# Kernel optimization log

Measured on AMD Instinct MI355X. Metric: run time of the kernel, lower is better.

## Reference

```python
import jax, jax.numpy as jnp
import numpy as np

DEPTH = 11  # tree depth -> depth+1 routing steps, n_nodes = 2**(DEPTH+1)-1 = 4095


def setup_inputs() -> dict:
    key = jax.random.key(0)
    k1, k2, k3 = jax.random.split(key, 3)
    B, D_in, D_out = 8192, 2048, 2048
    n_nodes = 2 ** (DEPTH + 1) - 1
    x = jax.random.normal(k1, (B, D_in), dtype=jnp.float32)
    # nn.Linear(input_width, n_nodes, bias=False).weight : (n_nodes, D_in)
    W_in = jax.random.normal(k2, (n_nodes, D_in), dtype=jnp.float32) / np.sqrt(D_in).astype(np.float32)
    # nn.Linear(n_nodes, output_width, bias=False).weight : (D_out, n_nodes)
    W_out = jax.random.normal(k3, (D_out, n_nodes), dtype=jnp.float32) / np.sqrt(n_nodes).astype(np.float32)
    return {"x": x, "W_in": W_in, "W_out": W_out}


def reference(x, W_in, W_out):
    B = x.shape[0]
    # Torch loop recomputes linear_in(x) every step; the result is identical each
    # iteration, so compute the (B, n_nodes) logits once and gather per depth step.
    logits_all = x @ W_in.T  # (B, n_nodes)

    def step(cur, _):
        # gather the logit of each sample's current tree node
        score = jnp.take_along_axis(logits_all, cur[:, None], axis=1)[:, 0]  # (B,)
        nxt = cur * 2 + (score >= 0).astype(jnp.int32) + 1  # left/right child
        return nxt, (cur, score)

    init = jnp.zeros((B,), dtype=jnp.int32)
    _, (nodes, scores) = jax.lax.scan(step, init, None, length=DEPTH + 1)
    nodes = nodes.T    # (B, depth+1) visited node ids
    scores = scores.T  # (B, depth+1) selected logits

    mlp1 = jax.nn.gelu(scores, approximate=False)  # exact GELU, matches nn.GELU
    # Conditional output projection: only the depth+1 visited columns of W_out
    # contribute per sample (FFF / conditional-MoE semantics).
    W_sel = W_out.T[nodes]  # (B, depth+1, D_out)
    return jnp.einsum('bd,bdo->bo', mlp1, W_sel)
```

## Files before the change

### kernel.cpp

```cpp
#include <hip/hip_runtime.h>
#include <math.h>

#define B_SZ     8192
#define D_IN     2048
#define D_OUT    2048
#define N_NODES  4095
#define STEPS    12
#define N_LEAVES 2048
#define N_SUB    512
#define CAP      64

typedef float f4_t __attribute__((ext_vector_type(4)));

__device__ __forceinline__ float4 nt_load4(const float* p) {
  f4_t v = __builtin_nontemporal_load((const f4_t*)p);
  return make_float4(v.x, v.y, v.z, v.w);
}

__global__ __launch_bounds__(256) void transpose_wout(
    const float* __restrict__ W, float* __restrict__ Wt) {
  __shared__ float tile[64][65];
  const int bx = blockIdx.x;
  const int tid = threadIdx.x;
  const int col0 = (bx & 63) * 64;
  const int row0 = (bx >> 6) * 64;
  const int r  = tid >> 4;
  const int c4 = (tid & 15) * 4;

  #pragma unroll
  for (int i = 0; i < 4; ++i) {
    const int row = r + i * 16;
    const float* src = W + (size_t)(row0 + row) * N_NODES + col0 + c4;
    if (col0 + c4 + 3 < N_NODES) {
      const float4 v = nt_load4(src);
      tile[c4 + 0][row] = v.x; tile[c4 + 1][row] = v.y;
      tile[c4 + 2][row] = v.z; tile[c4 + 3][row] = v.w;
    } else {
      #pragma unroll
      for (int k = 0; k < 4; ++k)
        tile[c4 + k][row] = (col0 + c4 + k < N_NODES) ? src[k] : 0.0f;
    }
  }
  __syncthreads();
  #pragma unroll
  for (int i = 0; i < 4; ++i) {
    const int rn = r + i * 16;
    const int node = col0 + rn;
    if (node < N_NODES) {
      float4 v;
      v.x = tile[rn][c4 + 0]; v.y = tile[rn][c4 + 1];
      v.z = tile[rn][c4 + 2]; v.w = tile[rn][c4 + 3];
      *(float4*)(Wt + (size_t)node * D_OUT + row0 + c4) = v;
    }
  }
}

__global__ __launch_bounds__(256) void route_kernel(
    const float* __restrict__ x, const float* __restrict__ W_in,
    int* __restrict__ cnt, int* __restrict__ bucket,
    float* __restrict__ gsc) {
  const int wave = (int)((blockIdx.x * (size_t)blockDim.x + threadIdx.x) >> 6);
  const int lane = threadIdx.x & 63;
  if (wave >= B_SZ) return;

  const float* xbase = x + (size_t)wave * D_IN;
  float4 xv0 = nt_load4(xbase + (lane + 0 * 64) * 4);
  float4 xv1 = nt_load4(xbase + (lane + 1 * 64) * 4);
  float4 xv2 = nt_load4(xbase + (lane + 2 * 64) * 4);
  float4 xv3 = nt_load4(xbase + (lane + 3 * 64) * 4);
  float4 xv4 = nt_load4(xbase + (lane + 4 * 64) * 4);
  float4 xv5 = nt_load4(xbase + (lane + 5 * 64) * 4);
  float4 xv6 = nt_load4(xbase + (lane + 6 * 64) * 4);
  float4 xv7 = nt_load4(xbase + (lane + 7 * 64) * 4);

  int cur = 0;
  #pragma unroll
  for (int d = 0; d < STEPS; ++d) {
    const float4* wr = (const float4*)(W_in + (size_t)cur * D_IN);
    const float4 w0 = wr[lane + 0 * 64];
    const float4 w1 = wr[lane + 1 * 64];
    const float4 w2 = wr[lane + 2 * 64];
    const float4 w3 = wr[lane + 3 * 64];
    const float4 w4 = wr[lane + 4 * 64];
    const float4 w5 = wr[lane + 5 * 64];
    const float4 w6 = wr[lane + 6 * 64];
    const float4 w7 = wr[lane + 7 * 64];
    float s = 0.0f;
    s += xv0.x * w0.x + xv0.y * w0.y + xv0.z * w0.z + xv0.w * w0.w;
    s += xv1.x * w1.x + xv1.y * w1.y + xv1.z * w1.z + xv1.w * w1.w;
    s += xv2.x * w2.x + xv2.y * w2.y + xv2.z * w2.z + xv2.w * w2.w;
    s += xv3.x * w3.x + xv3.y * w3.y + xv3.z * w3.z + xv3.w * w3.w;
    s += xv4.x * w4.x + xv4.y * w4.y + xv4.z * w4.z + xv4.w * w4.w;
    s += xv5.x * w5.x + xv5.y * w5.y + xv5.z * w5.z + xv5.w * w5.w;
    s += xv6.x * w6.x + xv6.y * w6.y + xv6.z * w6.z + xv6.w * w6.w;
    s += xv7.x * w7.x + xv7.y * w7.y + xv7.z * w7.z + xv7.w * w7.w;

    #pragma unroll
    for (int off = 32; off > 0; off >>= 1) s += __shfl_xor(s, off);

    if (lane == 0) {
      gsc[wave * STEPS + d] = 0.5f * s * (1.0f + erff(s * 0.70710678118654752f));
      if (d == STEPS - 1) {
        const int leaf = cur - 2047;
        const int pos = atomicAdd(&cnt[leaf], 1);
        if (pos < CAP) bucket[leaf * CAP + pos] = wave;
      }
    }
    cur = cur * 2 + ((s >= 0.0f) ? 2 : 1);
  }
}

__global__ __launch_bounds__(256) void out_kernel(
    const float* __restrict__ Wt, const int* __restrict__ cnt,
    const int* __restrict__ bucket, const float* __restrict__ gsc,
    float* __restrict__ out) {
  const int sub = blockIdx.x * 4 + (threadIdx.x >> 6);
  const int lane = threadIdx.x & 63;
  const int col = blockIdx.y * 64 + lane;

  int anc[10];
  {
    int nd = 511 + sub;
    #pragma unroll
    for (int d = 9; d >= 0; --d) { anc[d] = nd; nd = (nd - 1) >> 1; }
  }
  const int p10a = 1023 + 2 * sub;
  const int leaf0n = 2047 + 4 * sub;

  float wa[10], wp[2], wl[4];
  #pragma unroll
  for (int d = 0; d < 10; ++d)
    wa[d] = Wt[(size_t)anc[d] * D_OUT + col];
  #pragma unroll
  for (int k = 0; k < 2; ++k)
    wp[k] = Wt[(size_t)(p10a + k) * D_OUT + col];
  #pragma unroll
  for (int k = 0; k < 4; ++k)
    wl[k] = Wt[(size_t)(leaf0n + k) * D_OUT + col];

  int n0 = cnt[4 * sub + 0]; if (n0 > CAP) n0 = CAP;
  int n1 = cnt[4 * sub + 1]; if (n1 > CAP) n1 = CAP;
  int n2 = cnt[4 * sub + 2]; if (n2 > CAP) n2 = CAP;
  int n3 = cnt[4 * sub + 3]; if (n3 > CAP) n3 = CAP;
  const int p1 = n0, p2 = n0 + n1, p3 = n0 + n1 + n2;
  const int total = p3 + n3;

  for (int base = 0; base < total; base += 64) {
    const int m = (total - base < 64) ? (total - base) : 64;
    int packed = 0;
    {
      const int gi = base + lane;
      if (gi < total) {
        int lc, off;
        if      (gi < p1) { lc = 0; off = 0;  }
        else if (gi < p2) { lc = 1; off = p1; }
        else if (gi < p3) { lc = 2; off = p2; }
        else              { lc = 3; off = p3; }
        const int b = bucket[(4 * sub + lc) * CAP + (gi - off)];
        packed = (lc << 28) | b;
      }
    }
    int pA = __shfl(packed, 0);
    int pB = __shfl(packed, (m > 1) ? 1 : 0);
    const float4* gA = (const float4*)(gsc + (size_t)(pA & 0x0FFFFFFF) * STEPS);
    float4 a0 = gA[0], a1 = gA[1], a2 = gA[2];
    const float4* gB = (const float4*)(gsc + (size_t)(pB & 0x0FFFFFFF) * STEPS);
    float4 b0 = gB[0], b1 = gB[1], b2 = gB[2];

    for (int j = 0; j < m; ++j) {
      int jn = j + 2; if (jn >= m) jn = m - 1;
      const int pC = __shfl(packed, jn);
      const float4* gC = (const float4*)(gsc + (size_t)(pC & 0x0FFFFFFF) * STEPS);
      const float4 t0 = gC[0], t1 = gC[1], t2 = gC[2];

      const int b  = pA & 0x0FFFFFFF;
      const int lc = pA >> 28;
      const float w10 = (lc & 2) ? wp[1] : wp[0];
      const float w11 = (lc & 2) ? ((lc & 1) ? wl[3] : wl[2])
                                 : ((lc & 1) ? wl[1] : wl[0]);
      float acc;
      acc  = a0.x * wa[0];
      acc += a0.y * wa[1];
      acc += a0.z * wa[2];
      acc += a0.w * wa[3];
      acc += a1.x * wa[4];
      acc += a1.y * wa[5];
      acc += a1.z * wa[6];
      acc += a1.w * wa[7];
      acc += a2.x * wa[8];
      acc += a2.y * wa[9];
      acc += a2.z * w10;
      acc += a2.w * w11;
      __builtin_nontemporal_store(acc, out + (size_t)b * D_OUT + col);

      pA = pB; a0 = b0; a1 = b1; a2 = b2;
      pB = pC; b0 = t0; b1 = t1; b2 = t2;
    }
  }
}

extern "C" void kernel_launch(void* const* d_in, const int* in_sizes, int n_in,
                              void* d_out, int out_size, void* d_ws, size_t ws_size,
                              hipStream_t stream) {
  const float* x     = (const float*)d_in[0];
  const float* W_in  = (const float*)d_in[1];
  const float* W_out = (const float*)d_in[2];
  float* out = (float*)d_out;

  char* p = (char*)d_ws;
  float* Wt     = (float*)p;  p += (size_t)N_NODES * D_OUT * sizeof(float);
  int*   cnt    = (int*)p;    p += (size_t)N_LEAVES * sizeof(int);
  int*   bucket = (int*)p;    p += (size_t)N_LEAVES * CAP * sizeof(int);
  float* gsc    = (float*)p;

  hipMemsetAsync(cnt, 0, (size_t)N_LEAVES * sizeof(int), stream);

  route_kernel<<<dim3(B_SZ / 4), dim3(256), 0, stream>>>(
      x, W_in, cnt, bucket, gsc);

  transpose_wout<<<dim3(2048), dim3(256), 0, stream>>>(W_out, Wt);

  out_kernel<<<dim3(N_SUB / 4, 32), dim3(256), 0, stream>>>(
      Wt, cnt, bucket, gsc, out);
}
```

Measured before the change: 245.5 us.

## Vectorize out_kernel to four columns per lane and pin loads with asm barriers

The output kernel now has each lane handle four adjacent columns, using float4 weight loads and float4 nontemporal stores. This cuts the grid's y dimension by four and amortizes the per-sample gsc loads and shuffles over more work. The routing kernel gains a launch_bounds occupancy hint and empty asm barriers that force the x and W_in loads to be issued early. The transpose drops its nontemporal hint on W_out loads. The price is higher register pressure in out_kernel and fewer blocks overall.

```diff
diff --git a/kernel.cpp b/kernel.cpp
--- a/kernel.cpp
+++ b/kernel.cpp
@@ -10,11 +10,10 @@
 #define N_SUB    512
 #define CAP      64
 
-typedef float f4_t __attribute__((ext_vector_type(4)));
-
-__device__ __forceinline__ float4 nt_load4(const float* p) {
-  f4_t v = __builtin_nontemporal_load((const f4_t*)p);
-  return make_float4(v.x, v.y, v.z, v.w);
+typedef float f4 __attribute__((ext_vector_type(4)));
+
+__device__ __forceinline__ f4 nt_load(const float* p) {
+  return __builtin_nontemporal_load((const f4*)p);
 }
 
 __global__ __launch_bounds__(256) void transpose_wout(
@@ -32,7 +31,7 @@
     const int row = r + i * 16;
     const float* src = W + (size_t)(row0 + row) * N_NODES + col0 + c4;
     if (col0 + c4 + 3 < N_NODES) {
-      const float4 v = nt_load4(src);
+      const float4 v = *(const float4*)src;
       tile[c4 + 0][row] = v.x; tile[c4 + 1][row] = v.y;
       tile[c4 + 2][row] = v.z; tile[c4 + 3][row] = v.w;
     } else {
@@ -55,7 +54,7 @@
   }
 }
 
-__global__ __launch_bounds__(256) void route_kernel(
+__global__ __launch_bounds__(256, 5) void route_kernel(
     const float* __restrict__ x, const float* __restrict__ W_in,
     int* __restrict__ cnt, int* __restrict__ bucket,
     float* __restrict__ gsc) {
@@ -64,27 +63,31 @@
   if (wave >= B_SZ) return;
 
   const float* xbase = x + (size_t)wave * D_IN;
-  float4 xv0 = nt_load4(xbase + (lane + 0 * 64) * 4);
-  float4 xv1 = nt_load4(xbase + (lane + 1 * 64) * 4);
-  float4 xv2 = nt_load4(xbase + (lane + 2 * 64) * 4);
-  float4 xv3 = nt_load4(xbase + (lane + 3 * 64) * 4);
-  float4 xv4 = nt_load4(xbase + (lane + 4 * 64) * 4);
-  float4 xv5 = nt_load4(xbase + (lane + 5 * 64) * 4);
-  float4 xv6 = nt_load4(xbase + (lane + 6 * 64) * 4);
-  float4 xv7 = nt_load4(xbase + (lane + 7 * 64) * 4);
+  f4 xv0 = nt_load(xbase + (lane + 0 * 64) * 4);
+  f4 xv1 = nt_load(xbase + (lane + 1 * 64) * 4);
+  f4 xv2 = nt_load(xbase + (lane + 2 * 64) * 4);
+  f4 xv3 = nt_load(xbase + (lane + 3 * 64) * 4);
+  f4 xv4 = nt_load(xbase + (lane + 4 * 64) * 4);
+  f4 xv5 = nt_load(xbase + (lane + 5 * 64) * 4);
+  f4 xv6 = nt_load(xbase + (lane + 6 * 64) * 4);
+  f4 xv7 = nt_load(xbase + (lane + 7 * 64) * 4);
+  asm volatile("" : "+v"(xv0), "+v"(xv1), "+v"(xv2), "+v"(xv3),
+                    "+v"(xv4), "+v"(xv5), "+v"(xv6), "+v"(xv7));
 
   int cur = 0;
   #pragma unroll
   for (int d = 0; d < STEPS; ++d) {
-    const float4* wr = (const float4*)(W_in + (size_t)cur * D_IN);
-    const float4 w0 = wr[lane + 0 * 64];
-    const float4 w1 = wr[lane + 1 * 64];
-    const float4 w2 = wr[lane + 2 * 64];
-    const float4 w3 = wr[lane + 3 * 64];
-    const float4 w4 = wr[lane + 4 * 64];
-    const float4 w5 = wr[lane + 5 * 64];
-    const float4 w6 = wr[lane + 6 * 64];
-    const float4 w7 = wr[lane + 7 * 64];
+    const f4* wr = (const f4*)(W_in + (size_t)cur * D_IN);
+    f4 w0 = wr[lane + 0 * 64];
+    f4 w1 = wr[lane + 1 * 64];
+    f4 w2 = wr[lane + 2 * 64];
+    f4 w3 = wr[lane + 3 * 64];
+    f4 w4 = wr[lane + 4 * 64];
+    f4 w5 = wr[lane + 5 * 64];
+    f4 w6 = wr[lane + 6 * 64];
+    f4 w7 = wr[lane + 7 * 64];
+    asm volatile("" : "+v"(w0), "+v"(w1), "+v"(w2), "+v"(w3),
+                      "+v"(w4), "+v"(w5), "+v"(w6), "+v"(w7));
     float s = 0.0f;
     s += xv0.x * w0.x + xv0.y * w0.y + xv0.z * w0.z + xv0.w * w0.w;
     s += xv1.x * w1.x + xv1.y * w1.y + xv1.z * w1.z + xv1.w * w1.w;
@@ -116,7 +119,7 @@
     float* __restrict__ out) {
   const int sub = blockIdx.x * 4 + (threadIdx.x >> 6);
   const int lane = threadIdx.x & 63;
-  const int col = blockIdx.y * 64 + lane;
+  const int col = blockIdx.y * 256 + lane * 4;
 
   int anc[10];
   {
@@ -127,16 +130,26 @@
   const int p10a = 1023 + 2 * sub;
   const int leaf0n = 2047 + 4 * sub;
 
-  float wa[10], wp[2], wl[4];
-  #pragma unroll
-  for (int d = 0; d < 10; ++d)
-    wa[d] = Wt[(size_t)anc[d] * D_OUT + col];
-  #pragma unroll
-  for (int k = 0; k < 2; ++k)
-    wp[k] = Wt[(size_t)(p10a + k) * D_OUT + col];
-  #pragma unroll
-  for (int k = 0; k < 4; ++k)
-    wl[k] = Wt[(size_t)(leaf0n + k) * D_OUT + col];
+  f4 wa0 = *(const f4*)(Wt + (size_t)anc[0] * D_OUT + col);
+  f4 wa1 = *(const f4*)(Wt + (size_t)anc[1] * D_OUT + col);
+  f4 wa2 = *(const f4*)(Wt + (size_t)anc[2] * D_OUT + col);
+  f4 wa3 = *(const f4*)(Wt + (size_t)anc[3] * D_OUT + col);
+  f4 wa4 = *(const f4*)(Wt + (size_t)anc[4] * D_OUT + col);
+  f4 wa5 = *(const f4*)(Wt + (size_t)anc[5] * D_OUT + col);
+  f4 wa6 = *(const f4*)(Wt + (size_t)anc[6] * D_OUT + col);
+  f4 wa7 = *(const f4*)(Wt + (size_t)anc[7] * D_OUT + col);
+  f4 wa8 = *(const f4*)(Wt + (size_t)anc[8] * D_OUT + col);
+  f4 wa9 = *(const f4*)(Wt + (size_t)anc[9] * D_OUT + col);
+  f4 wp0 = *(const f4*)(Wt + (size_t)(p10a + 0) * D_OUT + col);
+  f4 wp1 = *(const f4*)(Wt + (size_t)(p10a + 1) * D_OUT + col);
+  f4 wl0 = *(const f4*)(Wt + (size_t)(leaf0n + 0) * D_OUT + col);
+  f4 wl1 = *(const f4*)(Wt + (size_t)(leaf0n + 1) * D_OUT + col);
+  f4 wl2 = *(const f4*)(Wt + (size_t)(leaf0n + 2) * D_OUT + col);
+  f4 wl3 = *(const f4*)(Wt + (size_t)(leaf0n + 3) * D_OUT + col);
+  asm volatile("" : "+v"(wa0), "+v"(wa1), "+v"(wa2), "+v"(wa3), "+v"(wa4),
+                    "+v"(wa5), "+v"(wa6), "+v"(wa7), "+v"(wa8), "+v"(wa9),
+                    "+v"(wp0), "+v"(wp1),
+                    "+v"(wl0), "+v"(wl1), "+v"(wl2), "+v"(wl3));
 
   int n0 = cnt[4 * sub + 0]; if (n0 > CAP) n0 = CAP;
   int n1 = cnt[4 * sub + 1]; if (n1 > CAP) n1 = CAP;
@@ -175,23 +188,35 @@
 
       const int b  = pA & 0x0FFFFFFF;
       const int lc = pA >> 28;
-      const float w10 = (lc & 2) ? wp[1] : wp[0];
-      const float w11 = (lc & 2) ? ((lc & 1) ? wl[3] : wl[2])
-                                 : ((lc & 1) ? wl[1] : wl[0]);
-      float acc;
-      acc  = a0.x * wa[0];
-      acc += a0.y * wa[1];
-      acc += a0.z * wa[2];
-      acc += a0.w * wa[3];
-      acc += a1.x * wa[4];
-      acc += a1.y * wa[5];
-      acc += a1.z * wa[6];
-      acc += a1.w * wa[7];
-      acc += a2.x * wa[8];
-      acc += a2.y * wa[9];
-      acc += a2.z * w10;
-      acc += a2.w * w11;
-      __builtin_nontemporal_store(acc, out + (size_t)b * D_OUT + col);
+      const f4 w10 = (lc & 2) ? wp1 : wp0;
+      const f4 w11 = (lc & 2) ? ((lc & 1) ? wl3 : wl2)
+                              : ((lc & 1) ? wl1 : wl0);
+      f4 acc;
+      acc.x = a0.x * wa0.x; acc.y = a0.x * wa0.y;
+      acc.z = a0.x * wa0.z; acc.w = a0.x * wa0.w;
+      acc.x += a0.y * wa1.x; acc.y += a0.y * wa1.y;
+      acc.z += a0.y * wa1.z; acc.w += a0.y * wa1.w;
+      acc.x += a0.z * wa2.x; acc.y += a0.z * wa2.y;
+      acc.z += a0.z * wa2.z; acc.w += a0.z * wa2.w;
+      acc.x += a0.w * wa3.x; acc.y += a0.w * wa3.y;
+      acc.z += a0.w * wa3.z; acc.w += a0.w * wa3.w;
+      acc.x += a1.x * wa4.x; acc.y += a1.x * wa4.y;
+      acc.z += a1.x * wa4.z; acc.w += a1.x * wa4.w;
+      acc.x += a1.y * wa5.x; acc.y += a1.y * wa5.y;
+      acc.z += a1.y * wa5.z; acc.w += a1.y * wa5.w;
+      acc.x += a1.z * wa6.x; acc.y += a1.z * wa6.y;
+      acc.z += a1.z * wa6.z; acc.w += a1.z * wa6.w;
+      acc.x += a1.w * wa7.x; acc.y += a1.w * wa7.y;
+      acc.z += a1.w * wa7.z; acc.w += a1.w * wa7.w;
+      acc.x += a2.x * wa8.x; acc.y += a2.x * wa8.y;
+      acc.z += a2.x * wa8.z; acc.w += a2.x * wa8.w;
+      acc.x += a2.y * wa9.x; acc.y += a2.y * wa9.y;
+      acc.z += a2.y * wa9.z; acc.w += a2.y * wa9.w;
+      acc.x += a2.z * w10.x; acc.y += a2.z * w10.y;
+      acc.z += a2.z * w10.z; acc.w += a2.z * w10.w;
+      acc.x += a2.w * w11.x; acc.y += a2.w * w11.y;
+      acc.z += a2.w * w11.z; acc.w += a2.w * w11.w;
+      __builtin_nontemporal_store(acc, (f4*)(out + (size_t)b * D_OUT + col));
 
       pA = pB; a0 = b0; a1 = b1; a2 = b2;
       pB = pC; b0 = t0; b1 = t1; b2 = t2;
@@ -220,6 +245,6 @@
 
   transpose_wout<<<dim3(2048), dim3(256), 0, stream>>>(W_out, Wt);
 
-  out_kernel<<<dim3(N_SUB / 4, 32), dim3(256), 0, stream>>>(
+  out_kernel<<<dim3(N_SUB / 4, 8), dim3(256), 0, stream>>>(
       Wt, cnt, bucket, gsc, out);
 }
```

Measured after the change: 220.0 us. 10.4% less time.
